# Performance work log

Measured on AMD Instinct MI355X. Metric: run time of the kernel, lower is better.

The kernel has to match this reference:

```python
import jax, jax.numpy as jnp
import numpy as np

HEADS = 32
HID = 4096
HD = HID // HEADS          # head_dim = 128
ROT = HD // 2              # rotary dim per stream = 64
SEQ = 2048


def _rope(x, pos):
    # x: [S, H, ROT]; pos: [S] int. GPT-NeoX-style interleaved pair rotation.
    d = x.shape[-1]
    inv_freq = 1.0 / (10000.0 ** (jnp.arange(0, d, 2, dtype=jnp.float32) / d))  # [d/2]
    ang = pos.astype(jnp.float32)[:, None] * inv_freq[None, :]                   # [S, d/2]
    cos = jnp.cos(ang)[:, None, :]
    sin = jnp.sin(ang)[:, None, :]
    xp = x.reshape(x.shape[0], x.shape[1], d // 2, 2)
    xe, xo = xp[..., 0], xp[..., 1]
    return jnp.stack([xe * cos - xo * sin, xe * sin + xo * cos], axis=-1).reshape(x.shape)


def setup_inputs() -> dict:
    key = jax.random.key(0)
    ks = jax.random.split(key, 6)
    return {
        "hidden_states": jax.random.normal(ks[0], (SEQ, HID), dtype=jnp.float32),
        "position_ids": jax.random.randint(ks[1], (2, SEQ), 0, SEQ),
        "W_qkv": jax.random.normal(ks[2], (HID, 3 * HID), dtype=jnp.float32) * 0.02,
        "b_qkv": jnp.zeros((3 * HID,), dtype=jnp.float32),
        "W_dense": jax.random.normal(ks[3], (HID, HID), dtype=jnp.float32) * 0.02,
        "b_dense": jnp.zeros((HID,), dtype=jnp.float32),
    }


def reference(hidden_states, position_ids, W_qkv, b_qkv, W_dense, b_dense):
    S = hidden_states.shape[0]
    # fused QKV projection; per-head packed layout [head][q|k|v]
    qkv = (hidden_states @ W_qkv + b_qkv).reshape(S, HEADS, 3, HD)
    q, k, v = qkv[:, :, 0], qkv[:, :, 1], qkv[:, :, 2]      # each [S, H, HD]
    p = position_ids[0] + 1
    b = position_ids[1] + 1
    def rot2(t):
        # 2D RoPE: first half rotated by position stream p, second by b
        return jnp.concatenate([_rope(t[..., :ROT], p), _rope(t[..., ROT:], b)], axis=-1)
    q = rot2(q)
    k = rot2(k)
    scale = 1.0 / jnp.sqrt(jnp.float32(HD))
    scores = jnp.einsum('shd,thd->hst', q, k) * scale        # [H, S, S]
    causal = jnp.tril(jnp.ones((S, S), dtype=bool))
    scores = jnp.where(causal[None], scores, jnp.float32(-1e9))
    attn = jax.nn.softmax(scores, axis=-1)
    ctx = jnp.einsum('hst,thd->shd', attn, v).reshape(S, HID)
    return ctx @ W_dense + b_dense
```

## Files before the change

### kernel.cpp

```cpp
#include <hip/hip_runtime.h>
#include <cstdint>
#include <cstdio>

typedef unsigned short u16;
typedef short bf16x8 __attribute__((ext_vector_type(8)));
typedef float f32x4 __attribute__((ext_vector_type(4)));
typedef unsigned short u16x8 __attribute__((ext_vector_type(8)));

#define SEQL 2048
#define NHEADS 32
#define HDIM 128
#define HIDDEN 4096

__device__ __forceinline__ u16 f2bf(float x){
  union { float f; unsigned u; } v; v.f = x;
  unsigned r = v.u + 0x7fffu + ((v.u >> 16) & 1u);
  return (u16)(r >> 16);
}
__device__ __forceinline__ float bf2f(u16 x){
  union { unsigned u; float f; } v; v.u = ((unsigned)x) << 16;
  return v.f;
}
__device__ __forceinline__ float exp2_asm(float x){
  float r; asm("v_exp_f32 %0, %1" : "=v"(r) : "v"(x)); return r;
}
__device__ __forceinline__ unsigned cvtpk_bf16(float lo, float hi){
  unsigned r; asm("v_cvt_pk_bf16_f32 %0, %1, %2" : "=v"(r) : "v"(lo), "v"(hi)); return r;
}

__device__ __forceinline__ void gload_lds16(const u16* g, u16* l){
  __builtin_amdgcn_global_load_lds((const __attribute__((address_space(1))) void*)g,
                                   (__attribute__((address_space(3))) void*)l, 16, 0, 0);
}

__global__ void cast_hs_kernel(const float* __restrict__ in, u16* __restrict__ out, int n8){
  int i = blockIdx.x * blockDim.x + threadIdx.x;
  if (i >= n8) return;
  const float4* p = (const float4*)in + (size_t)i*2;
  float4 a = p[0], b = p[1];
  u16x8 o;
  o[0]=f2bf(a.x); o[1]=f2bf(a.y); o[2]=f2bf(a.z); o[3]=f2bf(a.w);
  o[4]=f2bf(b.x); o[5]=f2bf(b.y); o[6]=f2bf(b.z); o[7]=f2bf(b.w);
  *((u16x8*)out + i) = o;
}

__global__ void wtrans_kernel(const float* __restrict__ W, u16* __restrict__ Wt,
                              int Ntot, int n0, int K){
  __shared__ float t[32][33];
  int tx = threadIdx.x, ty = threadIdx.y;
  int nn = blockIdx.x*32, k0 = blockIdx.y*32;
  #pragma unroll
  for (int i=0;i<4;i++)
    t[ty*4+i][tx] = W[(size_t)(k0+ty*4+i)*Ntot + n0 + nn + tx];
  __syncthreads();
  #pragma unroll
  for (int i=0;i<4;i++)
    Wt[(size_t)(nn+ty*4+i)*K + k0 + tx] = f2bf(t[tx][ty*4+i]);
}

template<int OUT_BF16>
__global__ __launch_bounds__(512) void gemm3_kernel(const u16* __restrict__ A, const u16* __restrict__ Bt,
                              const float* __restrict__ bias, void* __restrict__ Cv,
                              int K, int ldC, int NBM)
{
  extern __shared__ u16 lds[];
  int tid = threadIdx.x;
  int lane = tid & 63;
  int wave = tid >> 6;
  int lr = lane & 15, lg = lane >> 4;
  int wm = wave >> 2, wn = wave & 3;

  int nwg = gridDim.x;
  int cpx = nwg >> 3;
  int b0 = blockIdx.x;
  int swz = (b0 & 7) * cpx + (b0 >> 3);
  int bm = swz % NBM, bn = swz / NBM;
  int m0 = bm * 128, n0 = bn * 256;

  int NT = K >> 6;

  unsigned offA[2]; int ldsA[2];
  #pragma unroll
  for (int i=0;i<2;i++){
    int c = tid + i*512;
    int row = c >> 3, blk = c & 7;
    offA[i] = (unsigned)(m0 + row)*K + (unsigned)((blk ^ (row & 7))*8);
    ldsA[i] = c*8;
  }
  unsigned offB[4]; int ldsB[4];
  #pragma unroll
  for (int i=0;i<4;i++){
    int c = tid + i*512;
    int row = c >> 3, blk = c & 7;
    offB[i] = (unsigned)(n0 + row)*K + (unsigned)((blk ^ (row & 7))*8);
    ldsB[i] = c*8;
  }

  int colk[2];
  colk[0] = ((lg)     ^ (lr & 7))*8;
  colk[1] = ((4 + lg) ^ (lr & 7))*8;
  int rA[4], rB[4];
  #pragma unroll
  for (int m=0;m<4;m++) rA[m] = (wm*64 + m*16 + lr)*64;
  #pragma unroll
  for (int n=0;n<4;n++) rB[n] = (wn*64 + n*16 + lr)*64;

  f32x4 acc[4][4] = {};

  #pragma unroll
  for (int tt=0; tt<2; ++tt){
    u16* dA = lds + tt*24576;
    u16* dB = dA + 8192;
    int k0 = tt*64;
    #pragma unroll
    for (int i=0;i<2;i++) gload_lds16(A + offA[i] + k0, dA + ldsA[i]);
    #pragma unroll
    for (int i=0;i<4;i++) gload_lds16(Bt + offB[i] + k0, dB + ldsB[i]);
  }
  asm volatile("s_waitcnt vmcnt(6)" ::: "memory");
  asm volatile("s_barrier" ::: "memory");

  int p = 0, s2 = 2;
  for (int t = 0; t < NT; ++t){
    const u16* bA = lds + p*24576;
    const u16* bB = bA + 8192;
    u16* dA = lds + s2*24576;
    u16* dB = dA + 8192;
    bool st = (t + 2) < NT;
    int k2 = (t + 2) << 6;

    bf16x8 a_[4][2], bf0[2][2];
    #pragma unroll
    for (int m=0;m<4;m++){
      a_[m][0] = *(const bf16x8*)&bA[rA[m] + colk[0]];
      a_[m][1] = *(const bf16x8*)&bA[rA[m] + colk[1]];
    }
    #pragma unroll
    for (int n=0;n<2;n++){
      bf0[n][0] = *(const bf16x8*)&bB[rB[n] + colk[0]];
      bf0[n][1] = *(const bf16x8*)&bB[rB[n] + colk[1]];
    }
    if (st){
      gload_lds16(A + offA[0] + k2, dA + ldsA[0]);
      gload_lds16(A + offA[1] + k2, dA + ldsA[1]);
      gload_lds16(Bt + offB[0] + k2, dB + ldsB[0]);
    }
    asm volatile("s_barrier" ::: "memory");
    asm volatile("s_waitcnt lgkmcnt(0)" ::: "memory");
    __builtin_amdgcn_sched_barrier(0);
    __builtin_amdgcn_s_setprio(1);
    #pragma unroll
    for (int m=0;m<4;m++){
      #pragma unroll
      for (int n=0;n<2;n++){
        acc[m][n] = __builtin_amdgcn_mfma_f32_16x16x32_bf16(a_[m][0], bf0[n][0], acc[m][n], 0, 0, 0);
        acc[m][n] = __builtin_amdgcn_mfma_f32_16x16x32_bf16(a_[m][1], bf0[n][1], acc[m][n], 0, 0, 0);
      }
    }
    __builtin_amdgcn_s_setprio(0);
    asm volatile("s_barrier" ::: "memory");

    bf16x8 bf1[2][2];
    #pragma unroll
    for (int n=0;n<2;n++){
      bf1[n][0] = *(const bf16x8*)&bB[rB[n+2] + colk[0]];
      bf1[n][1] = *(const bf16x8*)&bB[rB[n+2] + colk[1]];
    }
    if (st){
      gload_lds16(Bt + offB[1] + k2, dB + ldsB[1]);
      gload_lds16(Bt + offB[2] + k2, dB + ldsB[2]);
      gload_lds16(Bt + offB[3] + k2, dB + ldsB[3]);
    }
    asm volatile("s_barrier" ::: "memory");
    asm volatile("s_waitcnt lgkmcnt(0)" ::: "memory");
    __builtin_amdgcn_sched_barrier(0);
    __builtin_amdgcn_s_setprio(1);
    #pragma unroll
    for (int m=0;m<4;m++){
      #pragma unroll
      for (int n=0;n<2;n++){
        acc[m][n+2] = __builtin_amdgcn_mfma_f32_16x16x32_bf16(a_[m][0], bf1[n][0], acc[m][n+2], 0, 0, 0);
        acc[m][n+2] = __builtin_amdgcn_mfma_f32_16x16x32_bf16(a_[m][1], bf1[n][1], acc[m][n+2], 0, 0, 0);
      }
    }
    __builtin_amdgcn_s_setprio(0);
    if (st) asm volatile("s_waitcnt vmcnt(6)" ::: "memory");
    else    asm volatile("s_waitcnt vmcnt(0)" ::: "memory");
    asm volatile("s_barrier" ::: "memory");

    p = (p == 2) ? 0 : p + 1;
    s2 = (s2 == 2) ? 0 : s2 + 1;
  }

  #pragma unroll
  for (int m=0;m<4;m++){
    #pragma unroll
    for (int n=0;n<4;n++){
      #pragma unroll
      for (int j=0;j<4;j++){
        int gr = m0 + wm*64 + m*16 + lg*4 + j;
        int gc = n0 + wn*64 + n*16 + lr;
        float v = acc[m][n][j] + bias[gc];
        if (OUT_BF16) ((u16*)Cv)[(size_t)gr*ldC + gc] = f2bf(v);
        else          ((float*)Cv)[(size_t)gr*ldC + gc] = v;
      }
    }
  }
}

__global__ __launch_bounds__(256) void rope_kernel(const u16* __restrict__ qkv, const int* __restrict__ pos,
                            u16* __restrict__ Q, u16* __restrict__ Kc, u16* __restrict__ V)
{
  int s = blockIdx.x*4 + (threadIdx.x >> 6);
  int h = blockIdx.y;
  int i = threadIdx.x & 63;
  int half = i >> 5, ii = i & 31;
  int d0 = half*64 + ii*2;
  const u16* base = qkv + (size_t)s*12288 + h*384;
  unsigned qp = *(const unsigned*)&base[d0];
  unsigned kp = *(const unsigned*)&base[128 + d0];
  unsigned vp = *(const unsigned*)&base[256 + d0];
  float qe = bf2f((u16)qp), qo = bf2f((u16)(qp >> 16));
  float ke = bf2f((u16)kp), ko = bf2f((u16)(kp >> 16));
  float pv = (float)(pos[half*SEQL + s] + 1);
  float fr = exp2f(-(float)ii * 0.4152410118609203f);
  float ang = pv * fr;
  float sn, cs; sincosf(ang, &sn, &cs);
  const float sc = 0.1275174313f;
  float q0 = (qe*cs - qo*sn)*sc, q1 = (qe*sn + qo*cs)*sc;
  float k0 = ke*cs - ko*sn,      k1 = ke*sn + ko*cs;
  size_t ob = ((size_t)h*SEQL + s)*HDIM + d0;
  *(unsigned*)&Q[ob]  = (unsigned)f2bf(q0) | ((unsigned)f2bf(q1) << 16);
  *(unsigned*)&Kc[ob] = (unsigned)f2bf(k0) | ((unsigned)f2bf(k1) << 16);
  *(unsigned*)&V[ob]  = vp;
}

__global__ void vtrans_kernel(const u16* __restrict__ V, u16* __restrict__ Vt){
  __shared__ u16 t[32][33];
  int h = blockIdx.z;
  int d0 = blockIdx.x*32, s0 = blockIdx.y*32;
  int tx = threadIdx.x, ty = threadIdx.y;
  const u16* Vh = V + (size_t)h*SEQL*HDIM;
  u16* Vth = Vt + (size_t)h*HDIM*SEQL;
  #pragma unroll
  for (int i=0;i<4;i++)
    t[ty*4+i][tx] = Vh[(size_t)(s0+ty*4+i)*HDIM + d0 + tx];
  __syncthreads();
  #pragma unroll
  for (int i=0;i<4;i++)
    Vth[(size_t)(d0+ty*4+i)*SEQL + s0 + tx] = t[tx][ty*4+i];
}

__global__ __launch_bounds__(256) void attn_kernel(const u16* __restrict__ Q, const u16* __restrict__ Kc,
                             const u16* __restrict__ Vt, u16* __restrict__ ctx)
{
  __shared__ u16 lK[2][64*128];
  __shared__ u16 lV[2][128*64];
  __shared__ u16 P[4*16*68];
  int qt = (gridDim.x - 1) - blockIdx.x;
  int h = blockIdx.y;
  int tid = threadIdx.x;
  int lane = tid & 63;
  int wave = tid >> 6;
  int lr = lane & 15, lg = lane >> 4;
  int q0a = qt*128 + wave*16;
  int q0b = q0a + 64;
  int qa = q0a + lr, qb = q0b + lr;
  const u16* Qh = Q  + (size_t)h*SEQL*HDIM;
  const u16* Kh = Kc + (size_t)h*SEQL*HDIM;
  const u16* Vh = Vt + (size_t)h*HDIM*SEQL;
  u16* Pw = &P[wave*1088];

  bf16x8 qfa[4], qfb[4];
  #pragma unroll
  for (int k32=0;k32<4;k32++){
    qfa[k32] = *(const bf16x8*)&Qh[(size_t)(q0a+lr)*HDIM + k32*32 + lg*8];
    qfb[k32] = *(const bf16x8*)&Qh[(size_t)(q0b+lr)*HDIM + k32*32 + lg*8];
  }

  f32x4 oa[8] = {}, ob[8] = {};
  float ma = -1e30f, la = 0.f;
  float mb = -1e30f, lb = 0.f;

  int nt = (qt+1)*2;

  #define STAGE64(BUF, T0) do {                                             \
    _Pragma("unroll")                                                       \
    for (int i=0;i<4;i++){                                                  \
      int c = i*256 + tid;                                                  \
      int row = c >> 4, b = c & 15;                                         \
      int bp = b ^ (row & 7);                                               \
      gload_lds16(Kh + (size_t)((T0) + row)*HDIM + bp*8, &lK[BUF][c*8]);    \
    }                                                                       \
    _Pragma("unroll")                                                       \
    for (int i=0;i<4;i++){                                                  \
      int c = i*256 + tid;                                                  \
      int dd = c >> 3, b = c & 7;                                           \
      int bp = b ^ (dd & 7);                                                \
      gload_lds16(Vh + (size_t)dd*SEQL + (T0) + bp*8, &lV[BUF][c*8]);       \
    }                                                                       \
  } while(0)

  #define SMAX(S4, O, MRUN, LRUN, QROW, Q0S, PA0, PA1) do {                 \
    float sv[16];                                                           \
    _Pragma("unroll")                                                       \
    for (int g=0;g<4;g++){                                                  \
      _Pragma("unroll")                                                     \
      for (int j=0;j<4;j++) sv[g*4+j] = S4[g][j];                           \
    }                                                                       \
    if (t0 + 63 > (Q0S)){             \
      int kb = t0 + lg*4;                                                   \
      _Pragma("unroll")                                                     \
      for (int g=0;g<4;g++){                                                \
        _Pragma("unroll")                                                   \
        for (int j=0;j<4;j++)                                               \
          sv[g*4+j] = (kb + g*16 + j > (QROW)) ? -1e30f : sv[g*4+j];        \
      }                                                                     \
    }                                                                       \
    float mx = fmaxf(                                                       \
      fmaxf(fmaxf(fmaxf(sv[0],sv[1]),fmaxf(sv[2],sv[3])),                   \
            fmaxf(fmaxf(sv[4],sv[5]),fmaxf(sv[6],sv[7]))),                  \
      fmaxf(fmaxf(fmaxf(sv[8],sv[9]),fmaxf(sv[10],sv[11])),                 \
            fmaxf(fmaxf(sv[12],sv[13]),fmaxf(sv[14],sv[15]))));             \
    mx = fmaxf(mx, __shfl_xor(mx, 16));                                     \
    mx = fmaxf(mx, __shfl_xor(mx, 32));                                     \
    if (!__all(mx <= (MRUN) + 11.5415603f)){                                \
      float mnew = fmaxf((MRUN), mx);                                       \
      float scl = exp2_asm((MRUN) - mnew);                                  \
      (LRUN) *= scl;                                                        \
      (MRUN) = mnew;                                                        \
      float sj[4];                                                          \
      _Pragma("unroll")                                                     \
      for (int j=0;j<4;j++) sj[j] = __shfl(scl, lg*4 + j);                  \
      _Pragma("unroll")                                                     \
      for (int n=0;n<8;n++){                                                \
        _Pragma("unroll")                                                   \
        for (int j=0;j<4;j++) O[n][j] *= sj[j];                             \
      }                                                                     \
    }                                                                       \
    float pr[16];                                                           \
    _Pragma("unroll")                                                       \
    for (int i=0;i<16;i++) pr[i] = exp2_asm(sv[i] - (MRUN));                \
    float sm = (((pr[0]+pr[1]) + (pr[2]+pr[3])) + ((pr[4]+pr[5]) + (pr[6]+pr[7]))) \
             + (((pr[8]+pr[9]) + (pr[10]+pr[11])) + ((pr[12]+pr[13]) + (pr[14]+pr[15]))); \
    sm += __shfl_xor(sm, 16);                                               \
    sm += __shfl_xor(sm, 32);                                               \
    (LRUN) += sm;                                                           \
    _Pragma("unroll")                                                       \
    for (int g=0;g<4;g++){                                                  \
      uint2 w;                                                              \
      w.x = cvtpk_bf16(pr[g*4],   pr[g*4+1]);                               \
      w.y = cvtpk_bf16(pr[g*4+2], pr[g*4+3]);                               \
      *(uint2*)&Pw[lr*68 + g*16 + lg*4] = w;                                \
    }                                                                       \
    PA0 = *(const bf16x8*)&Pw[lr*68 + lg*8];                                \
    PA1 = *(const bf16x8*)&Pw[lr*68 + 32 + lg*8];                           \
  } while(0)

  STAGE64(0, 0);
  __syncthreads();

  for (int t = 0; t < nt; ++t){
    int t0 = t*64;
    int cur = t & 1;
    if (t+1 < nt) STAGE64(cur^1, t0+64);

    const u16* Kt  = &lK[cur][0];
    const u16* Vtl = &lV[cur][0];
    bool ba = (t0 <= q0a + 15);

    f32x4 s4a[4] = {}, s4b[4] = {};
    if (ba){
      #pragma unroll
      for (int g=0; g<4; g++){
        int r = g*16 + lr;
        #pragma unroll
        for (int k32=0;k32<4;k32++){
          bf16x8 kf = *(const bf16x8*)&Kt[r*128 + ((((k32<<2)|lg) ^ (lr&7)))*8];
          s4a[g] = __builtin_amdgcn_mfma_f32_16x16x32_bf16(kf, qfa[k32], s4a[g], 0, 0, 0);
          s4b[g] = __builtin_amdgcn_mfma_f32_16x16x32_bf16(kf, qfb[k32], s4b[g], 0, 0, 0);
        }
      }
    } else {
      #pragma unroll
      for (int g=0; g<4; g++){
        int r = g*16 + lr;
        #pragma unroll
        for (int k32=0;k32<4;k32++){
          bf16x8 kf = *(const bf16x8*)&Kt[r*128 + ((((k32<<2)|lg) ^ (lr&7)))*8];
          s4b[g] = __builtin_amdgcn_mfma_f32_16x16x32_bf16(kf, qfb[k32], s4b[g], 0, 0, 0);
        }
      }
    }

    bf16x8 paa0, paa1, pab0, pab1;
    if (ba) SMAX(s4a, oa, ma, la, qa, q0a, paa0, paa1);
    SMAX(s4b, ob, mb, lb, qb, q0b, pab0, pab1);

    if (ba){
      #pragma unroll
      for (int n=0;n<8;n++){
        int dd = n*16 + lr;
        bf16x8 v0 = *(const bf16x8*)&Vtl[dd*64 + ((lg ^ (dd&7)))*8];
        bf16x8 v1 = *(const bf16x8*)&Vtl[dd*64 + (((4|lg) ^ (dd&7)))*8];
        oa[n] = __builtin_amdgcn_mfma_f32_16x16x32_bf16(paa0, v0, oa[n], 0, 0, 0);
        oa[n] = __builtin_amdgcn_mfma_f32_16x16x32_bf16(paa1, v1, oa[n], 0, 0, 0);
        ob[n] = __builtin_amdgcn_mfma_f32_16x16x32_bf16(pab0, v0, ob[n], 0, 0, 0);
        ob[n] = __builtin_amdgcn_mfma_f32_16x16x32_bf16(pab1, v1, ob[n], 0, 0, 0);
      }
    } else {
      #pragma unroll
      for (int n=0;n<8;n++){
        int dd = n*16 + lr;
        bf16x8 v0 = *(const bf16x8*)&Vtl[dd*64 + ((lg ^ (dd&7)))*8];
        bf16x8 v1 = *(const bf16x8*)&Vtl[dd*64 + (((4|lg) ^ (dd&7)))*8];
        ob[n] = __builtin_amdgcn_mfma_f32_16x16x32_bf16(pab0, v0, ob[n], 0, 0, 0);
        ob[n] = __builtin_amdgcn_mfma_f32_16x16x32_bf16(pab1, v1, ob[n], 0, 0, 0);
      }
    }
    __syncthreads();
  }
  #undef SMAX
  #undef STAGE64

  #pragma unroll
  for (int j=0;j<4;j++){
    float lja = __shfl(la, lg*4 + j);
    float inva = 1.f / lja;
    int srowa = q0a + lg*4 + j;
    #pragma unroll
    for (int n=0;n<8;n++)
      ctx[(size_t)srowa*HIDDEN + h*HDIM + n*16 + lr] = f2bf(oa[n][j]*inva);
    float ljb = __shfl(lb, lg*4 + j);
    float invb = 1.f / ljb;
    int srowb = q0b + lg*4 + j;
    #pragma unroll
    for (int n=0;n<8;n++)
      ctx[(size_t)srowb*HIDDEN + h*HDIM + n*16 + lr] = f2bf(ob[n][j]*invb);
  }
}

extern "C" void kernel_launch(void* const* d_in, const int* in_sizes, int n_in,
                              void* d_out, int out_size, void* d_ws, size_t ws_size,
                              hipStream_t stream)
{
  const float* hs   = (const float*)d_in[0];
  const int*   pos  = (const int*)d_in[1];
  const float* Wqkv = (const float*)d_in[2];
  const float* bqkv = (const float*)d_in[3];
  const float* Wd   = (const float*)d_in[4];
  const float* bd   = (const float*)d_in[5];

  const size_t o_hs  = 0;
  const size_t o_qkv = 16777216;
  const size_t o_Wtq = 67108864;
  const size_t o_Q   = 67108864;
  const size_t o_K   = 83886080;
  const size_t o_V   = 100663296;
  const size_t o_Vt  = 117440512;
  const size_t o_Wtd = 134217728;
  const size_t need  = 167772160;
  if (ws_size < need){
    fprintf(stderr, "kernel_launch: ws too small: %zu < %zu\n", ws_size, need);
    return;
  }
  char* w = (char*)d_ws;
  u16* hsb = (u16*)(w + o_hs);
  u16* qkv = (u16*)(w + o_qkv);
  u16* ctx = (u16*)(w + o_qkv);
  u16* Wtq = (u16*)(w + o_Wtq);
  u16* Qs  = (u16*)(w + o_Q);
  u16* Ks  = (u16*)(w + o_K);
  u16* Vs  = (u16*)(w + o_V);
  u16* Vts = (u16*)(w + o_Vt);
  u16* Wtd = (u16*)(w + o_Wtd);

  const size_t g3_lds = 3*24576*sizeof(u16);

  cast_hs_kernel<<<dim3(4096), dim3(256), 0, stream>>>(hs, hsb, SEQL*HIDDEN/8);
  wtrans_kernel<<<dim3(384,128), dim3(32,8), 0, stream>>>(Wqkv, Wtq, 12288, 0, 4096);

  gemm3_kernel<1><<<dim3(16*48), dim3(512), g3_lds, stream>>>(
      hsb, Wtq, bqkv, (void*)qkv, HIDDEN, 12288, 16);

  wtrans_kernel<<<dim3(128,128), dim3(32,8), 0, stream>>>(Wd, Wtd, 4096, 0, 4096);

  rope_kernel<<<dim3(SEQL/4, NHEADS), dim3(256), 0, stream>>>(qkv, pos, Qs, Ks, Vs);
  vtrans_kernel<<<dim3(4, 64, NHEADS), dim3(32,8), 0, stream>>>(Vs, Vts);
  attn_kernel<<<dim3(SEQL/128, NHEADS), dim3(256), 0, stream>>>(Qs, Ks, Vts, ctx);

  gemm3_kernel<0><<<dim3(16*16), dim3(512), g3_lds, stream>>>(
      ctx, Wtd, bd, d_out, HIDDEN, HIDDEN, 16);
}
```

Measured before the change: 504.4 us.

## Add 256x256-tile ping-pong GEMM for first two-thirds of QKV projection

Adds a new bf16 MFMA GEMM kernel with 256x256 output tiles, double-buffered LDS staging split into four quadrant phases with barriers, and setprio to interleave loads with MFMA. It computes the first 8192 columns of the QKV projection, and the existing gemm3 kernel handles the remaining 4096 columns. Larger tiles raise arithmetic intensity and cut global traffic per FLOP. The cost is two launches instead of one, high register pressure from 128 accumulator registers per thread, and a wave-quantization imbalance across the grid.

Measured after the change: 484.5 us. 1.04x faster.

```diff
diff --git a/kernel.cpp b/kernel.cpp
--- a/kernel.cpp
+++ b/kernel.cpp
@@ -56,6 +56,181 @@
   #pragma unroll
   for (int i=0;i<4;i++)
     Wt[(size_t)(nn+ty*4+i)*K + k0 + tx] = f2bf(t[tx][ty*4+i]);
+}
+
+template<int OUT_BF16>
+__global__ __launch_bounds__(512, 2) void gemm8_kernel(const u16* __restrict__ A, const u16* __restrict__ Bt,
+                              const float* __restrict__ bias, void* __restrict__ Cv,
+                              int K, int ldC)
+{
+  extern __shared__ u16 lds[];
+  int tid = threadIdx.x;
+  int lane = tid & 63;
+  int wave = tid >> 6;
+  int lr = lane & 15, lg = lane >> 4;
+  int wm = wave >> 2, wn = wave & 3;
+
+  int nwg = gridDim.x;
+  int cpx = nwg >> 3;
+  int b0 = blockIdx.x;
+  int swz = (b0 & 7) * cpx + (b0 >> 3);
+  int bm = swz & 7, bn = swz >> 3;
+  int m0 = bm * 256, n0 = bn * 256;
+  int NT = K >> 6;
+
+  int r0 = tid >> 3;
+  int cb0 = ((tid & 7) ^ (r0 & 7)) * 8;
+
+  const u16* A0p = A  + (size_t)m0*K;
+  const u16* A1p = A  + (size_t)(m0+128)*K;
+  const u16* B0p = Bt + (size_t)n0*K;
+  const u16* B1p = Bt + (size_t)(n0+128)*K;
+
+  #define STAGE8(G, SLOT) do {                                        \
+    gload_lds16((G) + (size_t)r0*K + cb0, lds + (SLOT) + tid*8);      \
+    gload_lds16((G) + (size_t)(r0+64)*K + cb0, lds + (SLOT) + (tid+512)*8); \
+  } while(0)
+
+  int x7 = lr & 7;
+  int colk0 = (lg ^ x7)*8;
+  int colk1 = ((4 + lg) ^ x7)*8;
+  int rA[4], rB[2];
+  #pragma unroll
+  for (int f=0; f<4; f++) rA[f] = (wm*64 + f*16 + lr)*64;
+  #pragma unroll
+  for (int nf=0; nf<2; nf++) rB[nf] = (wn*32 + nf*16 + lr)*64;
+
+  f32x4 acc[8][4] = {};
+  bf16x8 a_[4][2], b0r[2][2], b1r[2][2];
+
+  STAGE8(A0p,      0);
+  STAGE8(B0p,   8192);
+  STAGE8(B1p,  16384);
+  STAGE8(A1p,  24576);
+  STAGE8(A0p + 64, 32768);
+  STAGE8(B0p + 64, 40960);
+  STAGE8(B1p + 64, 49152);
+  asm volatile("s_waitcnt vmcnt(6)" ::: "memory");
+  asm volatile("s_barrier" ::: "memory");
+
+  for (int T = 0; T < NT; ++T){
+    int d = (T & 1) << 15;
+    int e = d ^ 32768;
+    const u16* sA0 = lds + d;
+    const u16* sB0 = lds + d + 8192;
+    const u16* sB1 = lds + d + 16384;
+    const u16* sA1 = lds + d + 24576;
+    int kc  = (T+1) << 6;
+    int kc2 = (T+2) << 6;
+    bool st2 = (T+2) < NT;
+
+    #pragma unroll
+    for (int f=0; f<4; f++){
+      a_[f][0] = *(const bf16x8*)&sA0[rA[f] + colk0];
+      a_[f][1] = *(const bf16x8*)&sA0[rA[f] + colk1];
+    }
+    #pragma unroll
+    for (int nf=0; nf<2; nf++){
+      b0r[nf][0] = *(const bf16x8*)&sB0[rB[nf] + colk0];
+      b0r[nf][1] = *(const bf16x8*)&sB0[rB[nf] + colk1];
+    }
+    if (T+1 < NT) STAGE8(A1p + kc, e + 24576);
+    asm volatile("s_barrier" ::: "memory");
+    asm volatile("s_waitcnt lgkmcnt(0)" ::: "memory");
+    __builtin_amdgcn_sched_barrier(0);
+    __builtin_amdgcn_s_setprio(1);
+    #pragma unroll
+    for (int f=0; f<4; f++){
+      #pragma unroll
+      for (int nf=0; nf<2; nf++){
+        acc[f][nf] = __builtin_amdgcn_mfma_f32_16x16x32_bf16(a_[f][0], b0r[nf][0], acc[f][nf], 0, 0, 0);
+        acc[f][nf] = __builtin_amdgcn_mfma_f32_16x16x32_bf16(a_[f][1], b0r[nf][1], acc[f][nf], 0, 0, 0);
+      }
+    }
+    __builtin_amdgcn_s_setprio(0);
+    asm volatile("s_barrier" ::: "memory");
+
+    #pragma unroll
+    for (int nf=0; nf<2; nf++){
+      b1r[nf][0] = *(const bf16x8*)&sB1[rB[nf] + colk0];
+      b1r[nf][1] = *(const bf16x8*)&sB1[rB[nf] + colk1];
+    }
+    if (st2) STAGE8(A0p + kc2, d);
+    asm volatile("s_barrier" ::: "memory");
+    asm volatile("s_waitcnt lgkmcnt(0)" ::: "memory");
+    __builtin_amdgcn_sched_barrier(0);
+    __builtin_amdgcn_s_setprio(1);
+    #pragma unroll
+    for (int f=0; f<4; f++){
+      #pragma unroll
+      for (int nf=0; nf<2; nf++){
+        acc[f][2+nf] = __builtin_amdgcn_mfma_f32_16x16x32_bf16(a_[f][0], b1r[nf][0], acc[f][2+nf], 0, 0, 0);
+        acc[f][2+nf] = __builtin_amdgcn_mfma_f32_16x16x32_bf16(a_[f][1], b1r[nf][1], acc[f][2+nf], 0, 0, 0);
+      }
+    }
+    __builtin_amdgcn_s_setprio(0);
+    asm volatile("s_barrier" ::: "memory");
+
+    #pragma unroll
+    for (int f=0; f<4; f++){
+      a_[f][0] = *(const bf16x8*)&sA1[rA[f] + colk0];
+      a_[f][1] = *(const bf16x8*)&sA1[rA[f] + colk1];
+    }
+    if (st2) STAGE8(B0p + kc2, d + 8192);
+    asm volatile("s_barrier" ::: "memory");
+    asm volatile("s_waitcnt lgkmcnt(0)" ::: "memory");
+    __builtin_amdgcn_sched_barrier(0);
+    __builtin_amdgcn_s_setprio(1);
+    #pragma unroll
+    for (int f=0; f<4; f++){
+      #pragma unroll
+      for (int nf=0; nf<2; nf++){
+        acc[4+f][2+nf] = __builtin_amdgcn_mfma_f32_16x16x32_bf16(a_[f][0], b1r[nf][0], acc[4+f][2+nf], 0, 0, 0);
+        acc[4+f][2+nf] = __builtin_amdgcn_mfma_f32_16x16x32_bf16(a_[f][1], b1r[nf][1], acc[4+f][2+nf], 0, 0, 0);
+      }
+    }
+    __builtin_amdgcn_s_setprio(0);
+    asm volatile("s_barrier" ::: "memory");
+
+    if (st2) STAGE8(B1p + kc2, d + 16384);
+    __builtin_amdgcn_s_setprio(1);
+    #pragma unroll
+    for (int f=0; f<4; f++){
+      #pragma unroll
+      for (int nf=0; nf<2; nf++){
+        acc[4+f][nf] = __builtin_amdgcn_mfma_f32_16x16x32_bf16(a_[f][0], b0r[nf][0], acc[4+f][nf], 0, 0, 0);
+        acc[4+f][nf] = __builtin_amdgcn_mfma_f32_16x16x32_bf16(a_[f][1], b0r[nf][1], acc[4+f][nf], 0, 0, 0);
+      }
+    }
+    __builtin_amdgcn_s_setprio(0);
+    if (T+1 < NT){
+      if (st2) asm volatile("s_waitcnt vmcnt(6)" ::: "memory");
+      else     asm volatile("s_waitcnt vmcnt(0)" ::: "memory");
+    }
+    asm volatile("s_barrier" ::: "memory");
+  }
+  #undef STAGE8
+
+  #pragma unroll
+  for (int mh=0; mh<2; mh++){
+    #pragma unroll
+    for (int f=0; f<4; f++){
+      #pragma unroll
+      for (int nh=0; nh<2; nh++){
+        #pragma unroll
+        for (int nf=0; nf<2; nf++){
+          #pragma unroll
+          for (int jj=0; jj<4; jj++){
+            int gr = m0 + mh*128 + wm*64 + f*16 + lg*4 + jj;
+            int gc = n0 + nh*128 + wn*32 + nf*16 + lr;
+            float v = acc[mh*4+f][nh*2+nf][jj] + bias[gc];
+            if (OUT_BF16) ((u16*)Cv)[(size_t)gr*ldC + gc] = f2bf(v);
+            else          ((float*)Cv)[(size_t)gr*ldC + gc] = v;
+          }
+        }
+      }
+    }
+  }
 }
 
 template<int OUT_BF16>
@@ -475,13 +650,17 @@
   u16* Vts = (u16*)(w + o_Vt);
   u16* Wtd = (u16*)(w + o_Wtd);
 
+  const size_t g8_lds = 65536*sizeof(u16);
   const size_t g3_lds = 3*24576*sizeof(u16);
 
   cast_hs_kernel<<<dim3(4096), dim3(256), 0, stream>>>(hs, hsb, SEQL*HIDDEN/8);
   wtrans_kernel<<<dim3(384,128), dim3(32,8), 0, stream>>>(Wqkv, Wtq, 12288, 0, 4096);
 
-  gemm3_kernel<1><<<dim3(16*48), dim3(512), g3_lds, stream>>>(
-      hsb, Wtq, bqkv, (void*)qkv, HIDDEN, 12288, 16);
+  gemm8_kernel<1><<<dim3(8*32), dim3(512), g8_lds, stream>>>(
+      hsb, Wtq, bqkv, (void*)qkv, HIDDEN, 12288);
+  gemm3_kernel<1><<<dim3(16*16), dim3(512), g3_lds, stream>>>(
+      hsb, Wtq + (size_t)8192*HIDDEN, bqkv + 8192, (void*)(qkv + 8192),
+      HIDDEN, 12288, 16);
 
   wtrans_kernel<<<dim3(128,128), dim3(32,8), 0, stream>>>(Wd, Wtd, 4096, 0, 4096);
 
```
